# Performance work log

Measured on AMD Instinct MI355X. Metric: run time of the kernel, lower is better.

The kernel has to match this reference:

```python
import jax, jax.numpy as jnp
import numpy as np

H = 16  # n_heads

def setup_inputs() -> dict:
    key = jax.random.key(0)
    ks = jax.random.split(key, 7)
    B, L, D = 4, 2048, 1024
    s = 0.02
    return {
        "z": jax.random.normal(ks[0], (B, L, D), jnp.float32),
        "connection": jax.random.normal(ks[1], (B, L, D), jnp.float32),
        "Wq": jax.random.normal(ks[2], (2 * D, D), jnp.float32) * s,
        "Wk": jax.random.normal(ks[3], (2 * D, D), jnp.float32) * s,
        "Wv": jax.random.normal(ks[4], (D, D), jnp.float32) * s,
        "Wo": jax.random.normal(ks[5], (D, D), jnp.float32) * s,
        "temp": jnp.float32(1.0),
    }

def reference(z, connection, Wq, Wk, Wv, Wo, temp):
    B, L, D = z.shape
    hd = D // H
    zc = jnp.concatenate([z, connection], axis=-1)          # [B,L,2D]
    Q = (zc @ Wq).reshape(B, L, H, hd).transpose(0, 2, 1, 3)  # [B,H,L,hd]
    K = (zc @ Wk).reshape(B, L, H, hd).transpose(0, 2, 1, 3)
    V = (z @ Wv).reshape(B, L, H, hd).transpose(0, 2, 1, 3)
    scale = (hd ** -0.5) * temp
    scores = jnp.einsum('bhqd,bhkd->bhqk', Q, K) * scale     # [B,H,L,L]
    rel = jax.nn.sigmoid(scores)
    rel_sum = jnp.clip(rel.sum(-1, keepdims=True), 1.0, None)
    out = jnp.einsum('bhqk,bhkd->bhqd', rel, V) / rel_sum
    out = out.transpose(0, 2, 1, 3).reshape(B, L, D)
    return out @ Wo
```

## Files before the change

kernel.cpp:

```cpp
#include <hip/hip_runtime.h>

typedef unsigned short u16;
typedef unsigned int u32;
typedef __bf16 bf16x8 __attribute__((ext_vector_type(8)));
typedef float f32x4 __attribute__((ext_vector_type(4)));

#define DEV static __device__ __forceinline__

DEV void gload16(const void* g, void* l) {
    __builtin_amdgcn_global_load_lds(
        (const __attribute__((address_space(1))) void*)g,
        (__attribute__((address_space(3))) void*)l, 16, 0, 0);
}

DEV void store_c(float* p, float v) { *p = v; }
DEV void store_c(u16* p, float v) { *(__bf16*)p = (__bf16)v; }

DEV int swz(int row, int bytecol) { return row * 128 + (bytecol ^ ((row & 7) << 4)); }

__global__ void pack_zc(const float* __restrict__ z, const float* __restrict__ cn,
                        u16* __restrict__ zc) {
    size_t i = ((size_t)blockIdx.x * blockDim.x + threadIdx.x) * 4;
    size_t t = i >> 11;
    int c = (int)(i & 2047);
    const float* src = (c < 1024) ? (z + t * 1024 + c) : (cn + t * 1024 + (c - 1024));
    float4 v = *reinterpret_cast<const float4*>(src);
    union { __bf16 h[4]; uint2 u; } o;
    o.h[0] = (__bf16)v.x; o.h[1] = (__bf16)v.y;
    o.h[2] = (__bf16)v.z; o.h[3] = (__bf16)v.w;
    *reinterpret_cast<uint2*>(zc + i) = o.u;
}

__global__ void transpose_conv_w(const float* __restrict__ W, u16* __restrict__ WT,
                                 int K, int N) {
    __shared__ float tile[32][33];
    int n0 = blockIdx.x * 32, k0 = blockIdx.y * 32;
    int tx = threadIdx.x, ty = threadIdx.y;
    #pragma unroll
    for (int i = ty; i < 32; i += 8)
        tile[i][tx] = W[(size_t)(k0 + i) * N + n0 + tx];
    __syncthreads();
    #pragma unroll
    for (int i = ty; i < 32; i += 8)
        *(__bf16*)&WT[(size_t)(n0 + i) * K + k0 + tx] = (__bf16)tile[tx][i];
}

__global__ void transpose_v(const u16* __restrict__ Vf, u16* __restrict__ Vt) {
    __shared__ u16 tile[32][33];
    int bh = blockIdx.z; int b = bh >> 4, h = bh & 15;
    int l0 = blockIdx.x * 32, d0 = blockIdx.y * 32;
    int tx = threadIdx.x, ty = threadIdx.y;
    #pragma unroll
    for (int i = ty; i < 32; i += 8)
        tile[i][tx] = Vf[(size_t)(b * 2048 + l0 + i) * 1024 + h * 64 + d0 + tx];
    __syncthreads();
    #pragma unroll
    for (int i = ty; i < 32; i += 8)
        Vt[((size_t)bh * 64 + d0 + i) * 2048 + l0 + tx] = tile[tx][i];
}

template <typename OutT>
__global__ __launch_bounds__(256, 2)
void gemm_bt(const u16* __restrict__ A, const u16* __restrict__ BT,
             OutT* __restrict__ C, int M, int N, int K,
             int lda, int ldb, int ldc) {
    __shared__ u16 As[128 * 64];
    __shared__ u16 Bs[128 * 64];
    const int tid = threadIdx.x;
    const int lane = tid & 63;
    const int wid = tid >> 6;
    const int m0 = blockIdx.x * 128;
    const int n0 = blockIdx.y * 128;
    const int wr = (wid >> 1) * 64;
    const int wc = (wid & 1) * 64;

    f32x4 acc[4][4];
    #pragma unroll
    for (int i = 0; i < 4; ++i)
        #pragma unroll
        for (int j = 0; j < 4; ++j)
            acc[i][j] = f32x4{0.f, 0.f, 0.f, 0.f};

    const int srcoff = ((lane & 7) ^ (lane >> 3)) * 8;
    const int rb = wid * 32 + (lane >> 3);
    const u16* aptr[4]; const u16* bptr[4];
    #pragma unroll
    for (int p = 0; p < 4; ++p) {
        aptr[p] = A  + (size_t)(m0 + rb + p * 8) * lda + srcoff;
        bptr[p] = BT + (size_t)(n0 + rb + p * 8) * ldb + srcoff;
    }

    for (int k0 = 0; k0 < K; k0 += 64) {
        __syncthreads();
        #pragma unroll
        for (int p = 0; p < 4; ++p)
            gload16(aptr[p] + k0, (char*)As + (wid * 4 + p) * 1024);
        #pragma unroll
        for (int p = 0; p < 4; ++p)
            gload16(bptr[p] + k0, (char*)Bs + (wid * 4 + p) * 1024);
        __syncthreads();

        #pragma unroll
        for (int kk = 0; kk < 64; kk += 32) {
            bf16x8 af[4], bfr[4];
            #pragma unroll
            for (int i = 0; i < 4; ++i) {
                int row = wr + i * 16 + (lane & 15);
                af[i] = *reinterpret_cast<const bf16x8*>(
                    reinterpret_cast<const char*>(As) + swz(row, (kk + (lane >> 4) * 8) * 2));
            }
            #pragma unroll
            for (int j = 0; j < 4; ++j) {
                int row = wc + j * 16 + (lane & 15);
                bfr[j] = *reinterpret_cast<const bf16x8*>(
                    reinterpret_cast<const char*>(Bs) + swz(row, (kk + (lane >> 4) * 8) * 2));
            }
            #pragma unroll
            for (int i = 0; i < 4; ++i)
                #pragma unroll
                for (int j = 0; j < 4; ++j)
                    acc[i][j] = __builtin_amdgcn_mfma_f32_16x16x32_bf16(af[i], bfr[j], acc[i][j], 0, 0, 0);
        }
    }

    #pragma unroll
    for (int i = 0; i < 4; ++i)
        #pragma unroll
        for (int j = 0; j < 4; ++j)
            #pragma unroll
            for (int r = 0; r < 4; ++r) {
                int row = m0 + wr + i * 16 + (lane >> 4) * 4 + r;
                int col = n0 + wc + j * 16 + (lane & 15);
                store_c(&C[(size_t)row * ldc + col], acc[i][j][r]);
            }
}

__global__ __launch_bounds__(256, 2)
void attn_kernel(const u16* __restrict__ QKf, const u16* __restrict__ Vt,
                 u16* __restrict__ Oa, const float* __restrict__ temp) {
    constexpr int L = 2048, D = 1024, QKLD = 2048, HD = 64;
    __shared__ u16 Qs[128 * 64];
    __shared__ u16 Ks[64 * 64];
    __shared__ u16 Vs[64 * 64];
    __shared__ u16 Ps[4][32 * 64];

    const int tid = threadIdx.x;
    const int lane = tid & 63;
    const int wid = tid >> 6;
    const int bh = blockIdx.y;
    const int b = bh >> 4, h = bh & 15;
    const int q0 = blockIdx.x * 128;
    const float sneg = -temp[0] * 0.125f * 1.44269504f;

    const u16* Qbase = QKf + (size_t)(b * L) * QKLD + h * HD;
    const u16* Kbase = Qbase + 1024;
    const u16* Vbase = Vt + (size_t)bh * HD * L;

    const int srcoff = ((lane & 7) ^ (lane >> 3)) * 8;

    #pragma unroll
    for (int p = 0; p < 4; ++p)
        gload16(Qbase + (size_t)(q0 + wid * 32 + p * 8 + (lane >> 3)) * QKLD + srcoff,
                (char*)Qs + (wid * 4 + p) * 1024);

    const int rb = wid * 16 + (lane >> 3);
    const u16* kptr[2]; const u16* vptr[2];
    #pragma unroll
    for (int p = 0; p < 2; ++p) {
        kptr[p] = Kbase + (size_t)(rb + p * 8) * QKLD + srcoff;
        vptr[p] = Vbase + (size_t)(rb + p * 8) * L + srcoff;
    }

    bf16x8 onesf;
    #pragma unroll
    for (int j = 0; j < 8; ++j) onesf[j] = (__bf16)1.0f;

    f32x4 oacc[4][2];
    #pragma unroll
    for (int ct = 0; ct < 4; ++ct)
        #pragma unroll
        for (int i = 0; i < 2; ++i) oacc[ct][i] = f32x4{0.f, 0.f, 0.f, 0.f};
    f32x4 racc[2];
    racc[0] = f32x4{0.f, 0.f, 0.f, 0.f};
    racc[1] = f32x4{0.f, 0.f, 0.f, 0.f};

    for (int k0 = 0; k0 < L; k0 += 64) {
        __syncthreads();
        #pragma unroll
        for (int p = 0; p < 2; ++p)
            gload16(kptr[p] + (size_t)k0 * QKLD, (char*)Ks + (wid * 2 + p) * 1024);
        #pragma unroll
        for (int p = 0; p < 2; ++p)
            gload16(vptr[p] + k0, (char*)Vs + (wid * 2 + p) * 1024);
        __syncthreads();

        f32x4 s[4][2];
        #pragma unroll
        for (int ct = 0; ct < 4; ++ct)
            #pragma unroll
            for (int i = 0; i < 2; ++i) s[ct][i] = f32x4{0.f, 0.f, 0.f, 0.f};
        #pragma unroll
        for (int kk = 0; kk < 64; kk += 32) {
            bf16x8 ak[4], bq[2];
            #pragma unroll
            for (int ct = 0; ct < 4; ++ct) {
                int krow = ct * 16 + (lane & 15);
                ak[ct] = *reinterpret_cast<const bf16x8*>(
                    reinterpret_cast<const char*>(Ks) + swz(krow, (kk + (lane >> 4) * 8) * 2));
            }
            #pragma unroll
            for (int i = 0; i < 2; ++i) {
                int qrow = wid * 32 + i * 16 + (lane & 15);
                bq[i] = *reinterpret_cast<const bf16x8*>(
                    reinterpret_cast<const char*>(Qs) + swz(qrow, (kk + (lane >> 4) * 8) * 2));
            }
            #pragma unroll
            for (int ct = 0; ct < 4; ++ct)
                #pragma unroll
                for (int i = 0; i < 2; ++i)
                    s[ct][i] = __builtin_amdgcn_mfma_f32_16x16x32_bf16(ak[ct], bq[i], s[ct][i], 0, 0, 0);
        }

        #pragma unroll
        for (int i = 0; i < 2; ++i) {
            int prow = i * 16 + (lane & 15);
            #pragma unroll
            for (int ct = 0; ct < 4; ++ct) {
                union { __bf16 hh[4]; uint2 uu; } pk;
                #pragma unroll
                for (int r = 0; r < 4; ++r)
                    pk.hh[r] = (__bf16)__builtin_amdgcn_rcpf(1.0f + exp2f(s[ct][i][r] * sneg));
                *reinterpret_cast<uint2*>(reinterpret_cast<char*>(Ps[wid]) +
                    swz(prow, ct * 32 + (lane >> 4) * 8)) = pk.uu;
            }
        }

        #pragma unroll
        for (int kk = 0; kk < 64; kk += 32) {
            bf16x8 ap[2];
            #pragma unroll
            for (int i = 0; i < 2; ++i) {
                int prow = i * 16 + (lane & 15);
                ap[i] = *reinterpret_cast<const bf16x8*>(
                    reinterpret_cast<const char*>(Ps[wid]) + swz(prow, (kk + (lane >> 4) * 8) * 2));
            }
            racc[0] = __builtin_amdgcn_mfma_f32_16x16x32_bf16(ap[0], onesf, racc[0], 0, 0, 0);
            racc[1] = __builtin_amdgcn_mfma_f32_16x16x32_bf16(ap[1], onesf, racc[1], 0, 0, 0);
            #pragma unroll
            for (int ct = 0; ct < 4; ++ct) {
                int vrow = ct * 16 + (lane & 15);
                bf16x8 bv = *reinterpret_cast<const bf16x8*>(
                    reinterpret_cast<const char*>(Vs) + swz(vrow, (kk + (lane >> 4) * 8) * 2));
                #pragma unroll
                for (int i = 0; i < 2; ++i)
                    oacc[ct][i] = __builtin_amdgcn_mfma_f32_16x16x32_bf16(ap[i], bv, oacc[ct][i], 0, 0, 0);
            }
        }
    }

    float rdiv[2][4];
    #pragma unroll
    for (int i = 0; i < 2; ++i)
        #pragma unroll
        for (int r = 0; r < 4; ++r)
            rdiv[i][r] = __builtin_amdgcn_rcpf(fmaxf(racc[i][r], 1.0f));

    #pragma unroll
    for (int ct = 0; ct < 4; ++ct)
        #pragma unroll
        for (int i = 0; i < 2; ++i)
            #pragma unroll
            for (int r = 0; r < 4; ++r) {
                int row = q0 + wid * 32 + i * 16 + (lane >> 4) * 4 + r;
                int col = h * HD + ct * 16 + (lane & 15);
                *(__bf16*)&Oa[(size_t)(b * L + row) * D + col] =
                    (__bf16)(oacc[ct][i][r] * rdiv[i][r]);
            }
}

extern "C" void kernel_launch(void* const* d_in, const int* in_sizes, int n_in,
                              void* d_out, int out_size, void* d_ws, size_t ws_size,
                              hipStream_t stream) {
    const float* z    = (const float*)d_in[0];
    const float* cn   = (const float*)d_in[1];
    const float* Wq   = (const float*)d_in[2];
    const float* Wk   = (const float*)d_in[3];
    const float* Wv   = (const float*)d_in[4];
    const float* Wo   = (const float*)d_in[5];
    const float* temp = (const float*)d_in[6];

    char* ws = (char*)d_ws;
    u16* zc  = (u16*)ws; ws += (size_t)8192 * 2048 * 2;
    u16* WqT = (u16*)ws; ws += (size_t)1024 * 2048 * 2;
    u16* WkT = (u16*)ws; ws += (size_t)1024 * 2048 * 2;
    u16* WvT = (u16*)ws; ws += (size_t)1024 * 1024 * 2;
    u16* WoT = (u16*)ws; ws += (size_t)1024 * 1024 * 2;
    u16* QKf = (u16*)ws; ws += (size_t)8192 * 2048 * 2;
    u16* Vf  = (u16*)ws; ws += (size_t)8192 * 1024 * 2;
    u16* Vt  = zc;
    u16* Oa  = Vf;

    pack_zc<<<16384, 256, 0, stream>>>(z, cn, zc);

    dim3 tb(32, 8);
    transpose_conv_w<<<dim3(32, 64), tb, 0, stream>>>(Wq, WqT, 2048, 1024);
    transpose_conv_w<<<dim3(32, 64), tb, 0, stream>>>(Wk, WkT, 2048, 1024);
    transpose_conv_w<<<dim3(32, 32), tb, 0, stream>>>(Wv, WvT, 1024, 1024);
    transpose_conv_w<<<dim3(32, 32), tb, 0, stream>>>(Wo, WoT, 1024, 1024);

    gemm_bt<u16><<<dim3(64, 16), 256, 0, stream>>>(zc, WqT, QKf, 8192, 2048, 2048, 2048, 2048, 2048);
    gemm_bt<u16><<<dim3(64, 8),  256, 0, stream>>>(zc, WvT, Vf,  8192, 1024, 1024, 2048, 1024, 1024);

    transpose_v<<<dim3(64, 2, 64), tb, 0, stream>>>(Vf, Vt);

    attn_kernel<<<dim3(16, 64), 256, 0, stream>>>(QKf, Vt, Oa, temp);

    gemm_bt<float><<<dim3(64, 8), 256, 0, stream>>>(Oa, WoT, (float*)d_out, 8192, 1024, 1024, 1024, 1024, 1024);
}
```

Baseline: 414.1 us.

## Double-buffer K/V tiles, keep Q in registers, remap blocks across XCDs

The attention kernel now double-buffers K/V tiles in LDS, prefetching the next tile while computing the current one, which leaves one barrier per iteration instead of two. Q fragments are loaded once into registers, removing the Q LDS buffer and its per-iteration reads. The P buffer uses an extra swizzle bit to reduce bank conflicts. Both GEMM and attention remap block IDs so neighbouring tiles share an XCD's L2. The trade-off is more register pressure and a larger LDS footprint for the K/V buffers.

```diff
diff --git a/kernel.cpp b/kernel.cpp
--- a/kernel.cpp
+++ b/kernel.cpp
@@ -17,6 +17,17 @@
 DEV void store_c(u16* p, float v) { *(__bf16*)p = (__bf16)v; }
 
 DEV int swz(int row, int bytecol) { return row * 128 + (bytecol ^ ((row & 7) << 4)); }
+DEV int swzP(int row, int bytecol) {
+    return row * 128 + (bytecol ^ ((row & 7) << 4) ^ (row & 8));
+}
+
+DEV void xcd_remap(int& bx, int& by, int gx, int gy) {
+    int nwg = gx * gy;
+    int bid = by * gx + bx;
+    int logical = (bid & 7) * (nwg >> 3) + (bid >> 3);
+    bx = logical % gx;
+    by = logical / gx;
+}
 
 __global__ void pack_zc(const float* __restrict__ z, const float* __restrict__ cn,
                         u16* __restrict__ zc) {
@@ -69,8 +80,10 @@
     const int tid = threadIdx.x;
     const int lane = tid & 63;
     const int wid = tid >> 6;
-    const int m0 = blockIdx.x * 128;
-    const int n0 = blockIdx.y * 128;
+    int bx = blockIdx.x, by = blockIdx.y;
+    xcd_remap(bx, by, gridDim.x, gridDim.y);
+    const int m0 = bx * 128;
+    const int n0 = by * 128;
     const int wr = (wid >> 1) * 64;
     const int wc = (wid & 1) * 64;
 
@@ -139,17 +152,19 @@
 void attn_kernel(const u16* __restrict__ QKf, const u16* __restrict__ Vt,
                  u16* __restrict__ Oa, const float* __restrict__ temp) {
     constexpr int L = 2048, D = 1024, QKLD = 2048, HD = 64;
-    __shared__ u16 Qs[128 * 64];
-    __shared__ u16 Ks[64 * 64];
-    __shared__ u16 Vs[64 * 64];
+    __shared__ u16 Ks[2][64 * 64];
+    __shared__ u16 Vs[2][64 * 64];
     __shared__ u16 Ps[4][32 * 64];
 
     const int tid = threadIdx.x;
     const int lane = tid & 63;
     const int wid = tid >> 6;
-    const int bh = blockIdx.y;
+    const int hi = lane >> 4;
+    int bx = blockIdx.x, by = blockIdx.y;
+    xcd_remap(bx, by, gridDim.x, gridDim.y);
+    const int bh = by;
     const int b = bh >> 4, h = bh & 15;
-    const int q0 = blockIdx.x * 128;
+    const int q0 = bx * 128;
     const float sneg = -temp[0] * 0.125f * 1.44269504f;
 
     const u16* Qbase = QKf + (size_t)(b * L) * QKLD + h * HD;
@@ -157,12 +172,6 @@
     const u16* Vbase = Vt + (size_t)bh * HD * L;
 
     const int srcoff = ((lane & 7) ^ (lane >> 3)) * 8;
-
-    #pragma unroll
-    for (int p = 0; p < 4; ++p)
-        gload16(Qbase + (size_t)(q0 + wid * 32 + p * 8 + (lane >> 3)) * QKLD + srcoff,
-                (char*)Qs + (wid * 4 + p) * 1024);
-
     const int rb = wid * 16 + (lane >> 3);
     const u16* kptr[2]; const u16* vptr[2];
     #pragma unroll
@@ -171,6 +180,21 @@
         vptr[p] = Vbase + (size_t)(rb + p * 8) * L + srcoff;
     }
 
+    bf16x8 qf[2][2];
+    #pragma unroll
+    for (int i = 0; i < 2; ++i)
+        #pragma unroll
+        for (int kx = 0; kx < 2; ++kx)
+            qf[i][kx] = *reinterpret_cast<const bf16x8*>(
+                Qbase + (size_t)(q0 + wid * 32 + i * 16 + (lane & 15)) * QKLD + kx * 32 + hi * 8);
+
+    #pragma unroll
+    for (int p = 0; p < 2; ++p)
+        gload16(kptr[p], (char*)Ks[0] + (wid * 2 + p) * 1024);
+    #pragma unroll
+    for (int p = 0; p < 2; ++p)
+        gload16(vptr[p], (char*)Vs[0] + (wid * 2 + p) * 1024);
+
     bf16x8 onesf;
     #pragma unroll
     for (int j = 0; j < 8; ++j) onesf[j] = (__bf16)1.0f;
@@ -184,15 +208,18 @@
     racc[0] = f32x4{0.f, 0.f, 0.f, 0.f};
     racc[1] = f32x4{0.f, 0.f, 0.f, 0.f};
 
+    __syncthreads();
+    int cur = 0;
+
     for (int k0 = 0; k0 < L; k0 += 64) {
-        __syncthreads();
-        #pragma unroll
-        for (int p = 0; p < 2; ++p)
-            gload16(kptr[p] + (size_t)k0 * QKLD, (char*)Ks + (wid * 2 + p) * 1024);
-        #pragma unroll
-        for (int p = 0; p < 2; ++p)
-            gload16(vptr[p] + k0, (char*)Vs + (wid * 2 + p) * 1024);
-        __syncthreads();
+        if (k0 + 64 < L) {
+            #pragma unroll
+            for (int p = 0; p < 2; ++p)
+                gload16(kptr[p] + (size_t)(k0 + 64) * QKLD, (char*)Ks[cur ^ 1] + (wid * 2 + p) * 1024);
+            #pragma unroll
+            for (int p = 0; p < 2; ++p)
+                gload16(vptr[p] + (k0 + 64), (char*)Vs[cur ^ 1] + (wid * 2 + p) * 1024);
+        }
 
         f32x4 s[4][2];
         #pragma unroll
@@ -200,25 +227,19 @@
             #pragma unroll
             for (int i = 0; i < 2; ++i) s[ct][i] = f32x4{0.f, 0.f, 0.f, 0.f};
         #pragma unroll
-        for (int kk = 0; kk < 64; kk += 32) {
-            bf16x8 ak[4], bq[2];
+        for (int kx = 0; kx < 2; ++kx) {
+            bf16x8 ak[4];
             #pragma unroll
             for (int ct = 0; ct < 4; ++ct) {
                 int krow = ct * 16 + (lane & 15);
                 ak[ct] = *reinterpret_cast<const bf16x8*>(
-                    reinterpret_cast<const char*>(Ks) + swz(krow, (kk + (lane >> 4) * 8) * 2));
-            }
-            #pragma unroll
-            for (int i = 0; i < 2; ++i) {
-                int qrow = wid * 32 + i * 16 + (lane & 15);
-                bq[i] = *reinterpret_cast<const bf16x8*>(
-                    reinterpret_cast<const char*>(Qs) + swz(qrow, (kk + (lane >> 4) * 8) * 2));
+                    reinterpret_cast<const char*>(Ks[cur]) + swz(krow, kx * 64 + hi * 16));
             }
             #pragma unroll
             for (int ct = 0; ct < 4; ++ct)
                 #pragma unroll
                 for (int i = 0; i < 2; ++i)
-                    s[ct][i] = __builtin_amdgcn_mfma_f32_16x16x32_bf16(ak[ct], bq[i], s[ct][i], 0, 0, 0);
+                    s[ct][i] = __builtin_amdgcn_mfma_f32_16x16x32_bf16(ak[ct], qf[i][kx], s[ct][i], 0, 0, 0);
         }
 
         #pragma unroll
@@ -231,18 +252,22 @@
                 for (int r = 0; r < 4; ++r)
                     pk.hh[r] = (__bf16)__builtin_amdgcn_rcpf(1.0f + exp2f(s[ct][i][r] * sneg));
                 *reinterpret_cast<uint2*>(reinterpret_cast<char*>(Ps[wid]) +
-                    swz(prow, ct * 32 + (lane >> 4) * 8)) = pk.uu;
-            }
-        }
-
-        #pragma unroll
-        for (int kk = 0; kk < 64; kk += 32) {
+                    swzP(prow, ct * 32 + hi * 8)) = pk.uu;
+            }
+        }
+
+        #pragma unroll
+        for (int kx = 0; kx < 2; ++kx) {
             bf16x8 ap[2];
             #pragma unroll
             for (int i = 0; i < 2; ++i) {
                 int prow = i * 16 + (lane & 15);
-                ap[i] = *reinterpret_cast<const bf16x8*>(
-                    reinterpret_cast<const char*>(Ps[wid]) + swz(prow, (kk + (lane >> 4) * 8) * 2));
+                union { u32 w[4]; bf16x8 v; } apu;
+                *reinterpret_cast<uint2*>(&apu.w[0]) = *reinterpret_cast<const uint2*>(
+                    reinterpret_cast<const char*>(Ps[wid]) + swzP(prow, kx * 64 + hi * 16));
+                *reinterpret_cast<uint2*>(&apu.w[2]) = *reinterpret_cast<const uint2*>(
+                    reinterpret_cast<const char*>(Ps[wid]) + swzP(prow, kx * 64 + hi * 16 + 8));
+                ap[i] = apu.v;
             }
             racc[0] = __builtin_amdgcn_mfma_f32_16x16x32_bf16(ap[0], onesf, racc[0], 0, 0, 0);
             racc[1] = __builtin_amdgcn_mfma_f32_16x16x32_bf16(ap[1], onesf, racc[1], 0, 0, 0);
@@ -250,12 +275,15 @@
             for (int ct = 0; ct < 4; ++ct) {
                 int vrow = ct * 16 + (lane & 15);
                 bf16x8 bv = *reinterpret_cast<const bf16x8*>(
-                    reinterpret_cast<const char*>(Vs) + swz(vrow, (kk + (lane >> 4) * 8) * 2));
+                    reinterpret_cast<const char*>(Vs[cur]) + swz(vrow, kx * 64 + hi * 16));
                 #pragma unroll
                 for (int i = 0; i < 2; ++i)
                     oacc[ct][i] = __builtin_amdgcn_mfma_f32_16x16x32_bf16(ap[i], bv, oacc[ct][i], 0, 0, 0);
             }
         }
+
+        __syncthreads();
+        cur ^= 1;
     }
 
     float rdiv[2][4];
@@ -271,7 +299,7 @@
         for (int i = 0; i < 2; ++i)
             #pragma unroll
             for (int r = 0; r < 4; ++r) {
-                int row = q0 + wid * 32 + i * 16 + (lane >> 4) * 4 + r;
+                int row = q0 + wid * 32 + i * 16 + hi * 4 + r;
                 int col = h * HD + ct * 16 + (lane & 15);
                 *(__bf16*)&Oa[(size_t)(b * L + row) * D + col] =
                     (__bf16)(oacc[ct][i][r] * rdiv[i][r]);
```

After: 410.4 us. No clear change (-0.9%).
